# Kernel tuning notes

Measured on AMD Instinct MI355X. Metric: run time of the kernel, lower is better.

## Reference

```python
import jax, jax.numpy as jnp
import numpy as np

B, S, HID = 1, 2048, 2048
H, KVH, HD = 16, 8, 128          # query heads, kv heads, head_dim = HID//H
N_REP = H // KVH                 # GQA expansion factor
EPS = 1e-6
THETA = 1e6
SCALING = HD ** (-0.5)           # note: original DIVIDES scores by this (bug kept)


def setup_inputs() -> dict:
    key = jax.random.key(0)
    ks = jax.random.split(key, 5)
    hidden_states = jax.random.normal(ks[0], (B, S, HID), jnp.float32)
    std = 0.02
    wq = jax.random.normal(ks[1], (HID, H * HD), jnp.float32) * std
    wk = jax.random.normal(ks[2], (HID, KVH * HD), jnp.float32) * std
    wv = jax.random.normal(ks[3], (HID, KVH * HD), jnp.float32) * std
    wo = jax.random.normal(ks[4], (H * HD, HID), jnp.float32) * std
    # RoPE tables as in Qwen3: inv_freq over even dims, emb = [freqs, freqs]
    pos = np.arange(S, dtype=np.float64)
    inv_freq = THETA ** (-np.arange(0, HD, 2, dtype=np.float64) / HD)
    freqs = pos[:, None] * inv_freq[None, :]            # [S, HD/2]
    emb = np.concatenate([freqs, freqs], axis=-1)       # [S, HD]
    cos = jnp.asarray(np.cos(emb)[None], jnp.float32)   # [1, S, HD]
    sin = jnp.asarray(np.sin(emb)[None], jnp.float32)
    return {"hidden_states": hidden_states, "cos": cos, "sin": sin,
            "wq": wq, "wk": wk, "wv": wv, "wo": wo}


def _rmsnorm(x):
    # weightless RMSNorm (the module's RMSNorm never applies .weight)
    return x * jax.lax.rsqrt(jnp.mean(x * x, axis=-1, keepdims=True) + EPS)


def _rotate_half(x):
    x1, x2 = jnp.split(x, 2, axis=-1)
    return jnp.concatenate([-x2, x1], axis=-1)


def reference(hidden_states, cos, sin, wq, wk, wv, wo):
    # projections + per-head QK RMSNorm, then [B,H,S,D] layout
    q = _rmsnorm((hidden_states @ wq).reshape(B, S, H, HD)).transpose(0, 2, 1, 3)
    k = _rmsnorm((hidden_states @ wk).reshape(B, S, KVH, HD)).transpose(0, 2, 1, 3)
    v = (hidden_states @ wv).reshape(B, S, KVH, HD).transpose(0, 2, 1, 3)
    # RoPE (cos/sin unsqueezed at head dim)
    c = cos[:, None, :, :]   # [B,1,S,HD]
    s = sin[:, None, :, :]
    q = q * c + _rotate_half(q) * s
    k = k * c + _rotate_half(k) * s
    # GQA repeat_kv: each kv head repeated N_REP consecutive times
    k = jnp.repeat(k, N_REP, axis=1)   # [B,H,S,HD]
    v = jnp.repeat(v, N_REP, axis=1)
    # faithful: scores DIVIDED by head_dim**-0.5 (i.e. * sqrt(HD)); no causal mask
    scores = jnp.einsum('bhqd,bhkd->bhqk', q, k) / SCALING
    probs = jax.nn.softmax(scores, axis=-1)
    attn = jnp.einsum('bhqk,bhkd->bhqd', probs, v)
    out = attn.transpose(0, 2, 1, 3).reshape(B, S, H * HD) @ wo
    return out
```

## Files before the change

kernel.cpp:

```cpp
#include <hip/hip_runtime.h>
#include <hip/hip_bf16.h>
#include <math.h>

#define S 2048
#define HID 2048
#define NH 16
#define KVH 8
#define HD 128
#define EPS 1e-6f
#define QK_SCALE 11.313708498984760390f

typedef __attribute__((ext_vector_type(8))) short s16x8;
typedef __attribute__((ext_vector_type(4))) float f32x4;

__device__ __forceinline__ unsigned short f2bf(float f) {
  __hip_bfloat16 h = __float2bfloat16(f);
  return *(unsigned short*)&h;
}
__device__ __forceinline__ float bf2f(unsigned short u) {
  unsigned int x = ((unsigned int)u) << 16;
  return __builtin_bit_cast(float, x);
}

__device__ __forceinline__ void gload16(const void* g, void* l) {
  __builtin_amdgcn_global_load_lds(
      (const __attribute__((address_space(1))) void*)g,
      (__attribute__((address_space(3))) void*)l, 16, 0, 0);
}

__global__ __launch_bounds__(256) void f32_to_bf16_split(const float* __restrict__ in,
                                                         unsigned short* __restrict__ hi,
                                                         unsigned short* __restrict__ lo,
                                                         int n4) {
  const int i = blockIdx.x * 256 + threadIdx.x;
  if (i < n4) {
    const float4 v = *(const float4*)(in + (size_t)i * 4);
    ushort4 h, l;
    h.x = f2bf(v.x); l.x = f2bf(v.x - bf2f(h.x));
    h.y = f2bf(v.y); l.y = f2bf(v.y - bf2f(h.y));
    h.z = f2bf(v.z); l.z = f2bf(v.z - bf2f(h.z));
    h.w = f2bf(v.w); l.w = f2bf(v.w - bf2f(h.w));
    *(ushort4*)(hi + (size_t)i * 4) = h;
    *(ushort4*)(lo + (size_t)i * 4) = l;
  }
}

__global__ __launch_bounds__(256) void transpose_to_bf16(const float* __restrict__ in,
                                                         unsigned short* __restrict__ out,
                                                         int K, int N) {
  __shared__ float t[64][65];
  const int n0 = blockIdx.x * 64;
  const int k0 = blockIdx.y * 64;
  const int tid = threadIdx.x;

  for (int idx = tid; idx < 64 * 16; idx += 256) {
    const int r = idx >> 4;
    const int c4 = (idx & 15) * 4;
    const float4 v = *(const float4*)(in + (size_t)(k0 + r) * N + n0 + c4);
    t[r][c4 + 0] = v.x; t[r][c4 + 1] = v.y; t[r][c4 + 2] = v.z; t[r][c4 + 3] = v.w;
  }
  __syncthreads();
  for (int idx = tid; idx < 64 * 16; idx += 256) {
    const int a = idx >> 4;
    const int b4 = (idx & 15) * 4;
    ushort4 u;
    u.x = f2bf(t[b4 + 0][a]); u.y = f2bf(t[b4 + 1][a]);
    u.z = f2bf(t[b4 + 2][a]); u.w = f2bf(t[b4 + 3][a]);
    *(ushort4*)(out + (size_t)(n0 + a) * K + k0 + b4) = u;
  }
}

__global__ __launch_bounds__(256) void transpose_to_bf16_split(const float* __restrict__ in,
                                                               unsigned short* __restrict__ ohi,
                                                               unsigned short* __restrict__ olo,
                                                               int K, int N) {
  __shared__ float t[64][65];
  const int n0 = blockIdx.x * 64;
  const int k0 = blockIdx.y * 64;
  const int tid = threadIdx.x;

  for (int idx = tid; idx < 64 * 16; idx += 256) {
    const int r = idx >> 4;
    const int c4 = (idx & 15) * 4;
    const float4 v = *(const float4*)(in + (size_t)(k0 + r) * N + n0 + c4);
    t[r][c4 + 0] = v.x; t[r][c4 + 1] = v.y; t[r][c4 + 2] = v.z; t[r][c4 + 3] = v.w;
  }
  __syncthreads();
  for (int idx = tid; idx < 64 * 16; idx += 256) {
    const int a = idx >> 4;
    const int b4 = (idx & 15) * 4;
    ushort4 h, l;
#pragma unroll
    for (int q = 0; q < 4; ++q) {
      const float v = t[b4 + q][a];
      const unsigned short hu = f2bf(v);
      const unsigned short lu = f2bf(v - bf2f(hu));
      ((unsigned short*)&h)[q] = hu;
      ((unsigned short*)&l)[q] = lu;
    }
    *(ushort4*)(ohi + (size_t)(n0 + a) * K + k0 + b4) = h;
    *(ushort4*)(olo + (size_t)(n0 + a) * K + k0 + b4) = l;
  }
}

#define BM 128
#define BN 128
#define BK 32

template <typename OT>
__global__ __launch_bounds__(256) void gemm_bf16_bt(const unsigned short* __restrict__ A,
                                                    const unsigned short* __restrict__ Bt,
                                                    OT* __restrict__ C,
                                                    int M, int N, int K, int ldc) {
  __shared__ unsigned short As[BM * BK];
  __shared__ unsigned short Bs[BN * BK];

  const int tid = threadIdx.x;
  const int lane = tid & 63;
  const int wave = tid >> 6;
  const int m0 = blockIdx.y * BM;
  const int n0 = blockIdx.x * BN;

  const int qm = (wave >> 1) * 64;
  const int qn = (wave & 1) * 64;
  const int l15 = lane & 15;
  const int quad = lane >> 4;

  const int st_row = lane >> 2;
  const int st_col = (lane & 3) * 8;

  f32x4 acc[4][4] = {};

  for (int k0 = 0; k0 < K; k0 += BK) {
#pragma unroll
    for (int p = 0; p < 2; ++p) {
      const int rb = p * 64 + wave * 16;
      gload16(A + (size_t)(m0 + rb + st_row) * K + k0 + st_col, &As[rb * BK]);
      gload16(Bt + (size_t)(n0 + rb + st_row) * K + k0 + st_col, &Bs[rb * BK]);
    }
    __syncthreads();

    s16x8 a[4], b[4];
#pragma unroll
    for (int i = 0; i < 4; ++i)
      a[i] = *(const s16x8*)&As[(qm + i * 16 + l15) * BK + quad * 8];
#pragma unroll
    for (int j = 0; j < 4; ++j)
      b[j] = *(const s16x8*)&Bs[(qn + j * 16 + l15) * BK + quad * 8];
#pragma unroll
    for (int i = 0; i < 4; ++i)
#pragma unroll
      for (int j = 0; j < 4; ++j)
        acc[i][j] = __builtin_amdgcn_mfma_f32_16x16x32_bf16(a[i], b[j], acc[i][j], 0, 0, 0);
    __syncthreads();
  }

#pragma unroll
  for (int i = 0; i < 4; ++i) {
    const int row_base = m0 + qm + i * 16 + quad * 4;
#pragma unroll
    for (int j = 0; j < 4; ++j) {
      const int col = n0 + qn + j * 16 + l15;
#pragma unroll
      for (int r = 0; r < 4; ++r) {
        if constexpr (sizeof(OT) == 2)
          C[(size_t)(row_base + r) * ldc + col] = (OT)f2bf(acc[i][j][r]);
        else
          C[(size_t)(row_base + r) * ldc + col] = acc[i][j][r];
      }
    }
  }
}

template <int MODE, typename OT>
__global__ __launch_bounds__(256) void gemm_bf16_bt64(const unsigned short* __restrict__ A,
                                                      const unsigned short* __restrict__ Bt,
                                                      OT* __restrict__ C,
                                                      int M, int N, int K, int ldc) {
  __shared__ unsigned short As[BM * BK];
  __shared__ unsigned short Bs[64 * BK];

  const int tid = threadIdx.x;
  const int lane = tid & 63;
  const int wave = tid >> 6;
  const int m0 = blockIdx.y * BM;
  const int n0 = blockIdx.x * 64;

  const int qm = (wave >> 1) * 64;
  const int qn = (wave & 1) * 32;
  const int l15 = lane & 15;
  const int quad = lane >> 4;

  const int st_row = lane >> 2;
  const int st_col = (lane & 3) * 8;

  f32x4 acc[4][2] = {};

  for (int k0 = 0; k0 < K; k0 += BK) {
#pragma unroll
    for (int p = 0; p < 2; ++p) {
      const int rb = p * 64 + wave * 16;
      gload16(A + (size_t)(m0 + rb + st_row) * K + k0 + st_col, &As[rb * BK]);
    }
    {
      const int rb = wave * 16;
      gload16(Bt + (size_t)(n0 + rb + st_row) * K + k0 + st_col, &Bs[rb * BK]);
    }
    __syncthreads();

    s16x8 a[4], b[2];
#pragma unroll
    for (int i = 0; i < 4; ++i)
      a[i] = *(const s16x8*)&As[(qm + i * 16 + l15) * BK + quad * 8];
#pragma unroll
    for (int j = 0; j < 2; ++j)
      b[j] = *(const s16x8*)&Bs[(qn + j * 16 + l15) * BK + quad * 8];
#pragma unroll
    for (int i = 0; i < 4; ++i)
#pragma unroll
      for (int j = 0; j < 2; ++j)
        acc[i][j] = __builtin_amdgcn_mfma_f32_16x16x32_bf16(a[i], b[j], acc[i][j], 0, 0, 0);
    __syncthreads();
  }

#pragma unroll
  for (int i = 0; i < 4; ++i) {
    const int row_base = m0 + qm + i * 16 + quad * 4;
#pragma unroll
    for (int j = 0; j < 2; ++j) {
      const int col = n0 + qn + j * 16 + l15;
      if constexpr (MODE == 0) {
#pragma unroll
        for (int r = 0; r < 4; ++r)
          C[(size_t)(row_base + r) * ldc + col] = acc[i][j][r];
      } else {
        ushort4 u;
        u.x = f2bf(acc[i][j][0]); u.y = f2bf(acc[i][j][1]);
        u.z = f2bf(acc[i][j][2]); u.w = f2bf(acc[i][j][3]);
        *(ushort4*)((unsigned short*)C + (size_t)col * ldc + row_base) = u;
      }
    }
  }
}

__global__ __launch_bounds__(256) void gemm_split_bt(const unsigned short* __restrict__ Ahi,
                                                     const unsigned short* __restrict__ Alo,
                                                     const unsigned short* __restrict__ Bhi,
                                                     const unsigned short* __restrict__ Blo,
                                                     float* __restrict__ C,
                                                     int M, int N, int K, int ldc) {
  __shared__ unsigned short AsH[BM * BK];
  __shared__ unsigned short AsL[BM * BK];
  __shared__ unsigned short BsH[BN * BK];
  __shared__ unsigned short BsL[BN * BK];

  const int tid = threadIdx.x;
  const int lane = tid & 63;
  const int wave = tid >> 6;
  const int m0 = blockIdx.y * BM;
  const int n0 = blockIdx.x * BN;

  const int qm = (wave >> 1) * 64;
  const int qn = (wave & 1) * 64;
  const int l15 = lane & 15;
  const int quad = lane >> 4;

  const int st_row = lane >> 2;
  const int st_col = (lane & 3) * 8;

  f32x4 acc[4][4] = {};

  for (int k0 = 0; k0 < K; k0 += BK) {
#pragma unroll
    for (int p = 0; p < 2; ++p) {
      const int rb = p * 64 + wave * 16;
      const size_t aoff = (size_t)(m0 + rb + st_row) * K + k0 + st_col;
      const size_t boff = (size_t)(n0 + rb + st_row) * K + k0 + st_col;
      gload16(Ahi + aoff, &AsH[rb * BK]);
      gload16(Alo + aoff, &AsL[rb * BK]);
      gload16(Bhi + boff, &BsH[rb * BK]);
      gload16(Blo + boff, &BsL[rb * BK]);
    }
    __syncthreads();

    s16x8 ah[4], al[4], bh[4], bl[4];
#pragma unroll
    for (int i = 0; i < 4; ++i) {
      const int ro = (qm + i * 16 + l15) * BK + quad * 8;
      ah[i] = *(const s16x8*)&AsH[ro];
      al[i] = *(const s16x8*)&AsL[ro];
    }
#pragma unroll
    for (int j = 0; j < 4; ++j) {
      const int ro = (qn + j * 16 + l15) * BK + quad * 8;
      bh[j] = *(const s16x8*)&BsH[ro];
      bl[j] = *(const s16x8*)&BsL[ro];
    }
#pragma unroll
    for (int i = 0; i < 4; ++i)
#pragma unroll
      for (int j = 0; j < 4; ++j) {
        acc[i][j] = __builtin_amdgcn_mfma_f32_16x16x32_bf16(ah[i], bh[j], acc[i][j], 0, 0, 0);
        acc[i][j] = __builtin_amdgcn_mfma_f32_16x16x32_bf16(ah[i], bl[j], acc[i][j], 0, 0, 0);
        acc[i][j] = __builtin_amdgcn_mfma_f32_16x16x32_bf16(al[i], bh[j], acc[i][j], 0, 0, 0);
      }
    __syncthreads();
  }

#pragma unroll
  for (int i = 0; i < 4; ++i) {
    const int row_base = m0 + qm + i * 16 + quad * 4;
#pragma unroll
    for (int j = 0; j < 4; ++j) {
      const int col = n0 + qn + j * 16 + l15;
#pragma unroll
      for (int r = 0; r < 4; ++r)
        C[(size_t)(row_base + r) * ldc + col] = acc[i][j][r];
    }
  }
}

__global__ __launch_bounds__(256) void rmsnorm_rope_split(const float* __restrict__ qk,
                                                          const float* __restrict__ cosb,
                                                          const float* __restrict__ sinb,
                                                          unsigned short* __restrict__ qh,
                                                          unsigned short* __restrict__ ql,
                                                          unsigned short* __restrict__ kh,
                                                          unsigned short* __restrict__ kl) {
  const int s = blockIdx.x;
  const int wave = threadIdx.x >> 6;
  const int lane = threadIdx.x & 63;
  const int hh = blockIdx.y * 4 + wave;
  const bool is_q = (hh < 16);
  const int col = is_q ? hh * HD : 2048 + (hh - 16) * HD;

  const float* row = qk + (size_t)s * 3072 + col;
  const float x1 = row[lane];
  const float x2 = row[lane + 64];

  float ss = x1 * x1 + x2 * x2;
  ss += __shfl_xor(ss, 1);
  ss += __shfl_xor(ss, 2);
  ss += __shfl_xor(ss, 4);
  ss += __shfl_xor(ss, 8);
  ss += __shfl_xor(ss, 16);
  ss += __shfl_xor(ss, 32);
  const float r = rsqrtf(ss / 128.f + EPS);

  const float c = cosb[(size_t)s * HD + lane];
  const float sn = sinb[(size_t)s * HD + lane];
  float o1 = x1 * r * c - x2 * r * sn;
  float o2 = x2 * r * c + x1 * r * sn;
  if (is_q) { o1 *= QK_SCALE; o2 *= QK_SCALE; }

  const unsigned short h1 = f2bf(o1), l1 = f2bf(o1 - bf2f(h1));
  const unsigned short h2 = f2bf(o2), l2 = f2bf(o2 - bf2f(h2));
  if (is_q) {
    const size_t base = (size_t)s * 2048 + hh * HD + lane;
    qh[base] = h1; ql[base] = l1;
    qh[base + 64] = h2; ql[base + 64] = l2;
  } else {
    const size_t base = (size_t)s * 1024 + (hh - 16) * HD + lane;
    kh[base] = h1; kl[base] = l1;
    kh[base + 64] = h2; kl[base + 64] = l2;
  }
}

#define FA_N 64

__global__ __launch_bounds__(256, 2) void attn_flash_mfma(const unsigned short* __restrict__ qh,
                                                          const unsigned short* __restrict__ ql,
                                                          const unsigned short* __restrict__ kh,
                                                          const unsigned short* __restrict__ kl,
                                                          const unsigned short* __restrict__ vt,
                                                          unsigned short* __restrict__ out) {
  const int h = blockIdx.y;
  const int kvh = h >> 1;
  const int m0 = blockIdx.x * 64;
  const int tid = threadIdx.x;
  const int lane = tid & 63;
  const int wave = tid >> 6;
  const int rg = wave >> 1;
  const int kg = wave & 1;
  const int l15 = lane & 15;
  const int quad = lane >> 4;

  __shared__ char smem[59392];
  unsigned short* Kh = (unsigned short*)(smem);
  unsigned short* Kl = (unsigned short*)(smem + 16384);
  unsigned short* Vt = (unsigned short*)(smem + 32768);
  unsigned short* Pt = (unsigned short*)(smem + 49152) + wave * 1280;

  s16x8 qah[2][4], qal[2][4];
#pragma unroll
  for (int rt = 0; rt < 2; ++rt) {
    const int qrow = m0 + rg * 32 + rt * 16 + l15;
#pragma unroll
    for (int ks = 0; ks < 4; ++ks) {
      const size_t off = (size_t)qrow * 2048 + h * HD + ks * 32 + quad * 8;
      qah[rt][ks] = *(const s16x8*)(qh + off);
      qal[rt][ks] = *(const s16x8*)(ql + off);
    }
  }

  f32x4 O[2][8] = {};
  float m_i[2][4], l_i[2][4];
#pragma unroll
  for (int rt = 0; rt < 2; ++rt)
#pragma unroll
    for (int r = 0; r < 4; ++r) { m_i[rt][r] = -1e30f; l_i[rt][r] = 0.f; }

  for (int n0 = 0; n0 < S; n0 += FA_N) {
    __syncthreads();
#pragma unroll
    for (int p = 0; p < 4; ++p) {
      const int krow = wave * 16 + p * 4 + (lane >> 4);
      const int kc = (lane & 15) ^ (krow & 15);
      const size_t ksrc = (size_t)(n0 + krow) * 1024 + kvh * HD + kc * 8;
      const int kdst = (wave * 16 + p * 4) * 128;
      gload16(kh + ksrc, Kh + kdst);
      gload16(kl + ksrc, Kl + kdst);
      const int d = wave * 32 + p * 8 + (lane >> 3);
      const int vc = (lane & 7) ^ (d & 7);
      const size_t vsrc = (size_t)(kvh * HD + d) * 2048 + n0 + vc * 8;
      const int vdst = (wave * 32 + p * 8) * 64;
      gload16(vt + vsrc, Vt + vdst);
    }
    __syncthreads();

    f32x4 sacc[2][2] = {};
#pragma unroll
    for (int ks = 0; ks < 4; ++ks) {
      s16x8 bh[2], bl[2];
#pragma unroll
      for (int j = 0; j < 2; ++j) {
        const int row = kg * 32 + j * 16 + l15;
        const int cp = ((ks * 4 + quad) ^ l15) * 8;
        const int ro = row * 128 + cp;
        bh[j] = *(const s16x8*)&Kh[ro];
        bl[j] = *(const s16x8*)&Kl[ro];
      }
#pragma unroll
      for (int rt = 0; rt < 2; ++rt)
#pragma unroll
        for (int j = 0; j < 2; ++j) {
          sacc[rt][j] = __builtin_amdgcn_mfma_f32_16x16x32_bf16(qah[rt][ks], bh[j], sacc[rt][j], 0, 0, 0);
          sacc[rt][j] = __builtin_amdgcn_mfma_f32_16x16x32_bf16(qah[rt][ks], bl[j], sacc[rt][j], 0, 0, 0);
          sacc[rt][j] = __builtin_amdgcn_mfma_f32_16x16x32_bf16(qal[rt][ks], bh[j], sacc[rt][j], 0, 0, 0);
        }
    }

#pragma unroll
    for (int rt = 0; rt < 2; ++rt) {
#pragma unroll
      for (int r = 0; r < 4; ++r) {
        float mt = fmaxf(sacc[rt][0][r], sacc[rt][1][r]);
        mt = fmaxf(mt, __shfl_xor(mt, 1));
        mt = fmaxf(mt, __shfl_xor(mt, 2));
        mt = fmaxf(mt, __shfl_xor(mt, 4));
        mt = fmaxf(mt, __shfl_xor(mt, 8));
        const float mnew = fmaxf(m_i[rt][r], mt);
        const float alpha = __expf(m_i[rt][r] - mnew);
        m_i[rt][r] = mnew;
        const float p0 = __expf(sacc[rt][0][r] - mnew);
        const float p1 = __expf(sacc[rt][1][r] - mnew);
        l_i[rt][r] = l_i[rt][r] * alpha + (p0 + p1);
#pragma unroll
        for (int jd = 0; jd < 8; ++jd) O[rt][jd][r] *= alpha;
        const int prow = rt * 16 + quad * 4 + r;
        Pt[prow * 40 + l15] = f2bf(p0);
        Pt[prow * 40 + 16 + l15] = f2bf(p1);
      }
    }

    s16x8 pa[2];
#pragma unroll
    for (int rt = 0; rt < 2; ++rt)
      pa[rt] = *(const s16x8*)&Pt[(rt * 16 + l15) * 40 + quad * 8];
#pragma unroll
    for (int jd = 0; jd < 8; ++jd) {
      const int d = jd * 16 + l15;
      const int cp = ((kg * 4 + quad) ^ (d & 7)) * 8;
      const s16x8 vb = *(const s16x8*)&Vt[d * 64 + cp];
#pragma unroll
      for (int rt = 0; rt < 2; ++rt)
        O[rt][jd] = __builtin_amdgcn_mfma_f32_16x16x32_bf16(pa[rt], vb, O[rt][jd], 0, 0, 0);
    }
  }

#pragma unroll
  for (int rt = 0; rt < 2; ++rt)
#pragma unroll
    for (int r = 0; r < 4; ++r) {
      float ls = l_i[rt][r];
      ls += __shfl_xor(ls, 1);
      ls += __shfl_xor(ls, 2);
      ls += __shfl_xor(ls, 4);
      ls += __shfl_xor(ls, 8);
      l_i[rt][r] = ls;
    }

  __syncthreads();
  float* Om = (float*)smem;
  float* ms = (float*)(smem + 32768);
  float* ls2 = (float*)(smem + 33024);

  if (kg == 1) {
#pragma unroll
    for (int rt = 0; rt < 2; ++rt)
#pragma unroll
      for (int r = 0; r < 4; ++r) {
        const int row = rt * 16 + quad * 4 + r;
        if (l15 == 0) {
          ms[rg * 32 + row] = m_i[rt][r];
          ls2[rg * 32 + row] = l_i[rt][r];
        }
#pragma unroll
        for (int jd = 0; jd < 8; ++jd)
          Om[(size_t)(rg * 32 + row) * 128 + jd * 16 + l15] = O[rt][jd][r];
      }
  }
  __syncthreads();
  if (kg == 0) {
#pragma unroll
    for (int rt = 0; rt < 2; ++rt)
#pragma unroll
      for (int r = 0; r < 4; ++r) {
        const int row = rt * 16 + quad * 4 + r;
        const float mB = ms[rg * 32 + row];
        const float lB = ls2[rg * 32 + row];
        const float mS = fmaxf(m_i[rt][r], mB);
        const float aA = __expf(m_i[rt][r] - mS);
        const float aB = __expf(mB - mS);
        const float inv = 1.f / (aA * l_i[rt][r] + aB * lB);
        const int grow = m0 + rg * 32 + row;
#pragma unroll
        for (int jd = 0; jd < 8; ++jd) {
          const float oB = Om[(size_t)(rg * 32 + row) * 128 + jd * 16 + l15];
          out[(size_t)grow * 2048 + h * HD + jd * 16 + l15] =
              f2bf((aA * O[rt][jd][r] + aB * oB) * inv);
        }
      }
  }
}

extern "C" void kernel_launch(void* const* d_in, const int* in_sizes, int n_in,
                              void* d_out, int out_size, void* d_ws, size_t ws_size,
                              hipStream_t stream) {
  const float* hidden = (const float*)d_in[0];
  const float* cosb   = (const float*)d_in[1];
  const float* sinb   = (const float*)d_in[2];
  const float* wq     = (const float*)d_in[3];
  const float* wk     = (const float*)d_in[4];
  const float* wv     = (const float*)d_in[5];
  const float* wo     = (const float*)d_in[6];
  float* out = (float*)d_out;

  char* w = (char*)d_ws;
  float* qk_buf           = (float*)(w);
  unsigned short* wqkT_hi = (unsigned short*)(w + (24u << 20));
  unsigned short* wqkT_lo = (unsigned short*)(w + (36u << 20));
  unsigned short* hid_hi  = (unsigned short*)(w + (48u << 20));
  unsigned short* hid_lo  = (unsigned short*)(w + (56u << 20));
  unsigned short* vt_b    = (unsigned short*)(w + (64u << 20));
  unsigned short* wvT     = (unsigned short*)(w + (68u << 20));
  unsigned short* q_hi    = (unsigned short*)(w + (24u << 20));
  unsigned short* q_lo    = (unsigned short*)(w + (32u << 20));
  unsigned short* k_hi    = (unsigned short*)(w + (40u << 20));
  unsigned short* k_lo    = (unsigned short*)(w + (44u << 20));
  unsigned short* woT     = (unsigned short*)(w + (48u << 20));
  unsigned short* a_b     = (unsigned short*)(w + (56u << 20));

  dim3 blk(256);

  f32_to_bf16_split<<<dim3((S * HID / 4 + 255) / 256), blk, 0, stream>>>(hidden, hid_hi, hid_lo, S * HID / 4);
  transpose_to_bf16_split<<<dim3(32, 32), blk, 0, stream>>>(wq, wqkT_hi, wqkT_lo, HID, 2048);
  transpose_to_bf16_split<<<dim3(16, 32), blk, 0, stream>>>(wk, wqkT_hi + (size_t)2048 * 2048,
                                                            wqkT_lo + (size_t)2048 * 2048, HID, 1024);
  transpose_to_bf16<<<dim3(16, 32), blk, 0, stream>>>(wv, wvT, 2048, 1024);

  gemm_split_bt<<<dim3(3072 / BN, S / BM), blk, 0, stream>>>(hid_hi, hid_lo, wqkT_hi, wqkT_lo,
                                                             qk_buf, S, 3072, HID, 3072);

  gemm_bf16_bt64<1, unsigned short><<<dim3(1024 / 64, S / BM), blk, 0, stream>>>(
      hid_hi, wvT, vt_b, S, 1024, HID, 2048);

  transpose_to_bf16<<<dim3(32, 32), blk, 0, stream>>>(wo, woT, 2048, HID);

  rmsnorm_rope_split<<<dim3(S, 6), blk, 0, stream>>>(qk_buf, cosb, sinb, q_hi, q_lo, k_hi, k_lo);

  attn_flash_mfma<<<dim3(S / 64, NH), blk, 0, stream>>>(q_hi, q_lo, k_hi, k_lo, vt_b, a_b);

  gemm_bf16_bt64<0, float><<<dim3(HID / 64, S / BM), blk, 0, stream>>>(
      a_b, woT, out, S, HID, 2048, HID);
}
```

Baseline: 420.3 us.

## Prefetch next K/V tile into registers, add lazy softmax rescale and MFMA priority

The flash-attention loop now loads the next K/V tile from global memory into registers while the current tile's QK and PV MFMAs run, then writes it to LDS after a barrier. This replaces the synchronous direct-to-LDS load at the top of each iteration. The online softmax skips the running-max update and the O/l rescale unless some row's max grows by more than 8, which saves exp and multiply work. s_setprio is raised around the MFMA blocks. The prefetch costs extra VGPRs for the staged tiles, which can lower occupancy, and the lazy rescale lets exponents grow by up to e^8 before renormalisation.

```diff
diff --git a/kernel.cpp b/kernel.cpp
--- a/kernel.cpp
+++ b/kernel.cpp
@@ -391,6 +391,11 @@
   unsigned short* Vt = (unsigned short*)(smem + 32768);
   unsigned short* Pt = (unsigned short*)(smem + 49152) + wave * 1280;
 
+  const int krow = wave * 16 + (lane >> 4);
+  const int kc = (lane & 15);
+  const int vd = wave * 32 + (lane >> 3);
+  const int vc7 = (lane & 7);
+
   s16x8 qah[2][4], qal[2][4];
 #pragma unroll
   for (int rt = 0; rt < 2; ++rt) {
@@ -410,25 +415,39 @@
 #pragma unroll
     for (int r = 0; r < 4; ++r) { m_i[rt][r] = -1e30f; l_i[rt][r] = 0.f; }
 
+#pragma unroll
+  for (int p = 0; p < 4; ++p) {
+    const int kr = krow + p * 4;
+    const size_t ksrc = (size_t)kr * 1024 + kvh * HD + (kc ^ (kr & 15)) * 8;
+    const int kdst = (wave * 16 + p * 4) * 128;
+    gload16(kh + ksrc, Kh + kdst);
+    gload16(kl + ksrc, Kl + kdst);
+    const int d = vd + p * 8;
+    const size_t vsrc = (size_t)(kvh * HD + d) * 2048 + (vc7 ^ (d & 7)) * 8;
+    const int vdst = (wave * 32 + p * 8) * 64;
+    gload16(vt + vsrc, Vt + vdst);
+  }
+  __syncthreads();
+
   for (int n0 = 0; n0 < S; n0 += FA_N) {
-    __syncthreads();
-#pragma unroll
-    for (int p = 0; p < 4; ++p) {
-      const int krow = wave * 16 + p * 4 + (lane >> 4);
-      const int kc = (lane & 15) ^ (krow & 15);
-      const size_t ksrc = (size_t)(n0 + krow) * 1024 + kvh * HD + kc * 8;
-      const int kdst = (wave * 16 + p * 4) * 128;
-      gload16(kh + ksrc, Kh + kdst);
-      gload16(kl + ksrc, Kl + kdst);
-      const int d = wave * 32 + p * 8 + (lane >> 3);
-      const int vc = (lane & 7) ^ (d & 7);
-      const size_t vsrc = (size_t)(kvh * HD + d) * 2048 + n0 + vc * 8;
-      const int vdst = (wave * 32 + p * 8) * 64;
-      gload16(vt + vsrc, Vt + vdst);
-    }
-    __syncthreads();
+    const int n1 = n0 + FA_N;
+
+    s16x8 stKh[4], stKl[4], stV[4];
+    if (n1 < S) {
+#pragma unroll
+      for (int p = 0; p < 4; ++p) {
+        const int kr = krow + p * 4;
+        const size_t ksrc = (size_t)(n1 + kr) * 1024 + kvh * HD + (kc ^ (kr & 15)) * 8;
+        stKh[p] = *(const s16x8*)(kh + ksrc);
+        stKl[p] = *(const s16x8*)(kl + ksrc);
+        const int d = vd + p * 8;
+        const size_t vsrc = (size_t)(kvh * HD + d) * 2048 + n1 + (vc7 ^ (d & 7)) * 8;
+        stV[p] = *(const s16x8*)(vt + vsrc);
+      }
+    }
 
     f32x4 sacc[2][2] = {};
+    __builtin_amdgcn_s_setprio(1);
 #pragma unroll
     for (int ks = 0; ks < 4; ++ks) {
       s16x8 bh[2], bl[2];
@@ -449,34 +468,52 @@
           sacc[rt][j] = __builtin_amdgcn_mfma_f32_16x16x32_bf16(qal[rt][ks], bh[j], sacc[rt][j], 0, 0, 0);
         }
     }
-
-#pragma unroll
-    for (int rt = 0; rt < 2; ++rt) {
+    __builtin_amdgcn_s_setprio(0);
+
+    float mt[2][4];
+    float dmax = -1e30f;
+#pragma unroll
+    for (int rt = 0; rt < 2; ++rt)
 #pragma unroll
       for (int r = 0; r < 4; ++r) {
-        float mt = fmaxf(sacc[rt][0][r], sacc[rt][1][r]);
-        mt = fmaxf(mt, __shfl_xor(mt, 1));
-        mt = fmaxf(mt, __shfl_xor(mt, 2));
-        mt = fmaxf(mt, __shfl_xor(mt, 4));
-        mt = fmaxf(mt, __shfl_xor(mt, 8));
-        const float mnew = fmaxf(m_i[rt][r], mt);
-        const float alpha = __expf(m_i[rt][r] - mnew);
-        m_i[rt][r] = mnew;
-        const float p0 = __expf(sacc[rt][0][r] - mnew);
-        const float p1 = __expf(sacc[rt][1][r] - mnew);
-        l_i[rt][r] = l_i[rt][r] * alpha + (p0 + p1);
-#pragma unroll
-        for (int jd = 0; jd < 8; ++jd) O[rt][jd][r] *= alpha;
+        float m = fmaxf(sacc[rt][0][r], sacc[rt][1][r]);
+        m = fmaxf(m, __shfl_xor(m, 1));
+        m = fmaxf(m, __shfl_xor(m, 2));
+        m = fmaxf(m, __shfl_xor(m, 4));
+        m = fmaxf(m, __shfl_xor(m, 8));
+        mt[rt][r] = m;
+        dmax = fmaxf(dmax, m - m_i[rt][r]);
+      }
+    if (__any(dmax > 8.f)) {
+#pragma unroll
+      for (int rt = 0; rt < 2; ++rt)
+#pragma unroll
+        for (int r = 0; r < 4; ++r) {
+          const float mnew = fmaxf(m_i[rt][r], mt[rt][r]);
+          const float alpha = __expf(m_i[rt][r] - mnew);
+          m_i[rt][r] = mnew;
+          l_i[rt][r] *= alpha;
+#pragma unroll
+          for (int jd = 0; jd < 8; ++jd) O[rt][jd][r] *= alpha;
+        }
+    }
+#pragma unroll
+    for (int rt = 0; rt < 2; ++rt)
+#pragma unroll
+      for (int r = 0; r < 4; ++r) {
+        const float p0 = __expf(sacc[rt][0][r] - m_i[rt][r]);
+        const float p1 = __expf(sacc[rt][1][r] - m_i[rt][r]);
+        l_i[rt][r] += p0 + p1;
         const int prow = rt * 16 + quad * 4 + r;
         Pt[prow * 40 + l15] = f2bf(p0);
         Pt[prow * 40 + 16 + l15] = f2bf(p1);
       }
-    }
 
     s16x8 pa[2];
 #pragma unroll
     for (int rt = 0; rt < 2; ++rt)
       pa[rt] = *(const s16x8*)&Pt[(rt * 16 + l15) * 40 + quad * 8];
+    __builtin_amdgcn_s_setprio(1);
 #pragma unroll
     for (int jd = 0; jd < 8; ++jd) {
       const int d = jd * 16 + l15;
@@ -485,6 +522,20 @@
 #pragma unroll
       for (int rt = 0; rt < 2; ++rt)
         O[rt][jd] = __builtin_amdgcn_mfma_f32_16x16x32_bf16(pa[rt], vb, O[rt][jd], 0, 0, 0);
+    }
+    __builtin_amdgcn_s_setprio(0);
+
+    if (n1 < S) {
+      __syncthreads();
+#pragma unroll
+      for (int p = 0; p < 4; ++p) {
+        const int kdst = (wave * 16 + p * 4) * 128 + lane * 8;
+        *(s16x8*)&Kh[kdst] = stKh[p];
+        *(s16x8*)&Kl[kdst] = stKl[p];
+        const int vdst = (wave * 32 + p * 8) * 64 + lane * 8;
+        *(s16x8*)&Vt[vdst] = stV[p];
+      }
+      __syncthreads();
     }
   }
 
```

After: 526.0 us. 25.1% more time.

## Double-buffer K/V tiles in flash attention with 8-wave blocks and lazy rescaling

Applied to the files above, without the earlier changes.

The attention kernel moves to 512-thread blocks in which each wave owns 16 query rows. K/V tiles are double-buffered in LDS so the next tile's global-to-LDS copy is issued right after a single barrier and overlaps the current tile's math. The online-softmax rescale of O and l is now skipped unless some row's running max grows by more than 8. MFMA sections are wrapped in s_setprio to favour matrix issue. The ~106 KB LDS footprint probably limits the CU to one block, and the deferred rescale lets unnormalised probabilities reach about e^8 before they are rounded to bf16.

```diff
diff --git a/kernel.cpp b/kernel.cpp
--- a/kernel.cpp
+++ b/kernel.cpp
@@ -367,8 +367,9 @@
 }
 
 #define FA_N 64
-
-__global__ __launch_bounds__(256, 2) void attn_flash_mfma(const unsigned short* __restrict__ qh,
+#define FA_NT (S / FA_N)
+
+__global__ __launch_bounds__(512, 2) void attn_flash_mfma(const unsigned short* __restrict__ qh,
                                                           const unsigned short* __restrict__ ql,
                                                           const unsigned short* __restrict__ kh,
                                                           const unsigned short* __restrict__ kl,
@@ -385,120 +386,126 @@
   const int l15 = lane & 15;
   const int quad = lane >> 4;
 
-  __shared__ char smem[59392];
-  unsigned short* Kh = (unsigned short*)(smem);
-  unsigned short* Kl = (unsigned short*)(smem + 16384);
-  unsigned short* Vt = (unsigned short*)(smem + 32768);
-  unsigned short* Pt = (unsigned short*)(smem + 49152) + wave * 1280;
-
-  s16x8 qah[2][4], qal[2][4];
-#pragma unroll
-  for (int rt = 0; rt < 2; ++rt) {
-    const int qrow = m0 + rg * 32 + rt * 16 + l15;
+  __shared__ char smem[108544];
+  unsigned short* Pt = (unsigned short*)(smem + 98304) + wave * 640;
+
+  auto STAGE = [&](int nt, int buf) {
+    unsigned short* KhB = (unsigned short*)(smem + buf * 49152);
+    unsigned short* KlB = KhB + 8192;
+    unsigned short* VtB = KhB + 16384;
+#pragma unroll
+    for (int p = 0; p < 2; ++p) {
+      const int kr = wave * 8 + p * 4 + (lane >> 4);
+      const size_t ksrc = (size_t)(nt + kr) * 1024 + kvh * HD + ((lane & 15) ^ (kr & 15)) * 8;
+      gload16(kh + ksrc, KhB + (wave * 8 + p * 4) * 128);
+      gload16(kl + ksrc, KlB + (wave * 8 + p * 4) * 128);
+      const int d = wave * 16 + p * 8 + (lane >> 3);
+      const size_t vsrc = (size_t)(kvh * HD + d) * 2048 + nt + ((lane & 7) ^ (d & 7)) * 8;
+      gload16(vt + vsrc, VtB + (wave * 16 + p * 8) * 64);
+    }
+  };
+
+  s16x8 qah[4], qal[4];
+  {
+    const int qrow = m0 + rg * 16 + l15;
 #pragma unroll
     for (int ks = 0; ks < 4; ++ks) {
       const size_t off = (size_t)qrow * 2048 + h * HD + ks * 32 + quad * 8;
-      qah[rt][ks] = *(const s16x8*)(qh + off);
-      qal[rt][ks] = *(const s16x8*)(ql + off);
-    }
-  }
-
-  f32x4 O[2][8] = {};
-  float m_i[2][4], l_i[2][4];
-#pragma unroll
-  for (int rt = 0; rt < 2; ++rt)
-#pragma unroll
-    for (int r = 0; r < 4; ++r) { m_i[rt][r] = -1e30f; l_i[rt][r] = 0.f; }
-
-  for (int n0 = 0; n0 < S; n0 += FA_N) {
-    __syncthreads();
-#pragma unroll
-    for (int p = 0; p < 4; ++p) {
-      const int krow = wave * 16 + p * 4 + (lane >> 4);
-      const int kc = (lane & 15) ^ (krow & 15);
-      const size_t ksrc = (size_t)(n0 + krow) * 1024 + kvh * HD + kc * 8;
-      const int kdst = (wave * 16 + p * 4) * 128;
-      gload16(kh + ksrc, Kh + kdst);
-      gload16(kl + ksrc, Kl + kdst);
-      const int d = wave * 32 + p * 8 + (lane >> 3);
-      const int vc = (lane & 7) ^ (d & 7);
-      const size_t vsrc = (size_t)(kvh * HD + d) * 2048 + n0 + vc * 8;
-      const int vdst = (wave * 32 + p * 8) * 64;
-      gload16(vt + vsrc, Vt + vdst);
-    }
-    __syncthreads();
-
-    f32x4 sacc[2][2] = {};
+      qah[ks] = *(const s16x8*)(qh + off);
+      qal[ks] = *(const s16x8*)(ql + off);
+    }
+  }
+
+  f32x4 O[8] = {};
+  float m_i[4], l_i[4];
+#pragma unroll
+  for (int r = 0; r < 4; ++r) { m_i[r] = -1e30f; l_i[r] = 0.f; }
+
+  STAGE(0, 0);
+
+  for (int t = 0; t < FA_NT; ++t) {
+    unsigned short* Kh = (unsigned short*)(smem + (t & 1) * 49152);
+    unsigned short* Kl = Kh + 8192;
+    unsigned short* Vt = Kh + 16384;
+
+    __syncthreads();
+    if (t + 1 < FA_NT) STAGE((t + 1) * FA_N, (t + 1) & 1);
+
+    f32x4 sacc[2] = {};
+    __builtin_amdgcn_s_setprio(1);
 #pragma unroll
     for (int ks = 0; ks < 4; ++ks) {
       s16x8 bh[2], bl[2];
 #pragma unroll
       for (int j = 0; j < 2; ++j) {
         const int row = kg * 32 + j * 16 + l15;
-        const int cp = ((ks * 4 + quad) ^ l15) * 8;
-        const int ro = row * 128 + cp;
+        const int ro = row * 128 + (((ks * 4 + quad) ^ l15) * 8);
         bh[j] = *(const s16x8*)&Kh[ro];
         bl[j] = *(const s16x8*)&Kl[ro];
       }
 #pragma unroll
-      for (int rt = 0; rt < 2; ++rt)
-#pragma unroll
-        for (int j = 0; j < 2; ++j) {
-          sacc[rt][j] = __builtin_amdgcn_mfma_f32_16x16x32_bf16(qah[rt][ks], bh[j], sacc[rt][j], 0, 0, 0);
-          sacc[rt][j] = __builtin_amdgcn_mfma_f32_16x16x32_bf16(qah[rt][ks], bl[j], sacc[rt][j], 0, 0, 0);
-          sacc[rt][j] = __builtin_amdgcn_mfma_f32_16x16x32_bf16(qal[rt][ks], bh[j], sacc[rt][j], 0, 0, 0);
-        }
-    }
-
-#pragma unroll
-    for (int rt = 0; rt < 2; ++rt) {
+      for (int j = 0; j < 2; ++j) {
+        sacc[j] = __builtin_amdgcn_mfma_f32_16x16x32_bf16(qah[ks], bh[j], sacc[j], 0, 0, 0);
+        sacc[j] = __builtin_amdgcn_mfma_f32_16x16x32_bf16(qah[ks], bl[j], sacc[j], 0, 0, 0);
+        sacc[j] = __builtin_amdgcn_mfma_f32_16x16x32_bf16(qal[ks], bh[j], sacc[j], 0, 0, 0);
+      }
+    }
+    __builtin_amdgcn_s_setprio(0);
+
+    float mt[4];
+    float dmax = -1e30f;
+#pragma unroll
+    for (int r = 0; r < 4; ++r) {
+      float m = fmaxf(sacc[0][r], sacc[1][r]);
+      m = fmaxf(m, __shfl_xor(m, 1));
+      m = fmaxf(m, __shfl_xor(m, 2));
+      m = fmaxf(m, __shfl_xor(m, 4));
+      m = fmaxf(m, __shfl_xor(m, 8));
+      mt[r] = m;
+      dmax = fmaxf(dmax, m - m_i[r]);
+    }
+    if (__any(dmax > 8.f)) {
 #pragma unroll
       for (int r = 0; r < 4; ++r) {
-        float mt = fmaxf(sacc[rt][0][r], sacc[rt][1][r]);
-        mt = fmaxf(mt, __shfl_xor(mt, 1));
-        mt = fmaxf(mt, __shfl_xor(mt, 2));
-        mt = fmaxf(mt, __shfl_xor(mt, 4));
-        mt = fmaxf(mt, __shfl_xor(mt, 8));
-        const float mnew = fmaxf(m_i[rt][r], mt);
-        const float alpha = __expf(m_i[rt][r] - mnew);
-        m_i[rt][r] = mnew;
-        const float p0 = __expf(sacc[rt][0][r] - mnew);
-        const float p1 = __expf(sacc[rt][1][r] - mnew);
-        l_i[rt][r] = l_i[rt][r] * alpha + (p0 + p1);
-#pragma unroll
-        for (int jd = 0; jd < 8; ++jd) O[rt][jd][r] *= alpha;
-        const int prow = rt * 16 + quad * 4 + r;
-        Pt[prow * 40 + l15] = f2bf(p0);
-        Pt[prow * 40 + 16 + l15] = f2bf(p1);
-      }
-    }
-
-    s16x8 pa[2];
-#pragma unroll
-    for (int rt = 0; rt < 2; ++rt)
-      pa[rt] = *(const s16x8*)&Pt[(rt * 16 + l15) * 40 + quad * 8];
+        const float mnew = fmaxf(m_i[r], mt[r]);
+        const float alpha = __expf(m_i[r] - mnew);
+        m_i[r] = mnew;
+        l_i[r] *= alpha;
+#pragma unroll
+        for (int jd = 0; jd < 8; ++jd) O[jd][r] *= alpha;
+      }
+    }
+#pragma unroll
+    for (int r = 0; r < 4; ++r) {
+      const float p0 = __expf(sacc[0][r] - m_i[r]);
+      const float p1 = __expf(sacc[1][r] - m_i[r]);
+      l_i[r] += p0 + p1;
+      const int prow = quad * 4 + r;
+      Pt[prow * 40 + l15] = f2bf(p0);
+      Pt[prow * 40 + 16 + l15] = f2bf(p1);
+    }
+
+    const s16x8 pa = *(const s16x8*)&Pt[l15 * 40 + quad * 8];
+    __builtin_amdgcn_s_setprio(1);
 #pragma unroll
     for (int jd = 0; jd < 8; ++jd) {
       const int d = jd * 16 + l15;
       const int cp = ((kg * 4 + quad) ^ (d & 7)) * 8;
       const s16x8 vb = *(const s16x8*)&Vt[d * 64 + cp];
-#pragma unroll
-      for (int rt = 0; rt < 2; ++rt)
-        O[rt][jd] = __builtin_amdgcn_mfma_f32_16x16x32_bf16(pa[rt], vb, O[rt][jd], 0, 0, 0);
-    }
-  }
-
-#pragma unroll
-  for (int rt = 0; rt < 2; ++rt)
-#pragma unroll
-    for (int r = 0; r < 4; ++r) {
-      float ls = l_i[rt][r];
-      ls += __shfl_xor(ls, 1);
-      ls += __shfl_xor(ls, 2);
-      ls += __shfl_xor(ls, 4);
-      ls += __shfl_xor(ls, 8);
-      l_i[rt][r] = ls;
-    }
+      O[jd] = __builtin_amdgcn_mfma_f32_16x16x32_bf16(pa, vb, O[jd], 0, 0, 0);
+    }
+    __builtin_amdgcn_s_setprio(0);
+  }
+
+#pragma unroll
+  for (int r = 0; r < 4; ++r) {
+    float ls = l_i[r];
+    ls += __shfl_xor(ls, 1);
+    ls += __shfl_xor(ls, 2);
+    ls += __shfl_xor(ls, 4);
+    ls += __shfl_xor(ls, 8);
+    l_i[r] = ls;
+  }
 
   __syncthreads();
   float* Om = (float*)smem;
@@ -507,40 +514,33 @@
 
   if (kg == 1) {
 #pragma unroll
-    for (int rt = 0; rt < 2; ++rt)
-#pragma unroll
-      for (int r = 0; r < 4; ++r) {
-        const int row = rt * 16 + quad * 4 + r;
-        if (l15 == 0) {
-          ms[rg * 32 + row] = m_i[rt][r];
-          ls2[rg * 32 + row] = l_i[rt][r];
-        }
-#pragma unroll
-        for (int jd = 0; jd < 8; ++jd)
-          Om[(size_t)(rg * 32 + row) * 128 + jd * 16 + l15] = O[rt][jd][r];
-      }
+    for (int r = 0; r < 4; ++r) {
+      const int row = rg * 16 + quad * 4 + r;
+      if (l15 == 0) { ms[row] = m_i[r]; ls2[row] = l_i[r]; }
+#pragma unroll
+      for (int jd = 0; jd < 8; ++jd)
+        Om[(size_t)row * 128 + jd * 16 + l15] = O[jd][r];
+    }
   }
   __syncthreads();
   if (kg == 0) {
 #pragma unroll
-    for (int rt = 0; rt < 2; ++rt)
-#pragma unroll
-      for (int r = 0; r < 4; ++r) {
-        const int row = rt * 16 + quad * 4 + r;
-        const float mB = ms[rg * 32 + row];
-        const float lB = ls2[rg * 32 + row];
-        const float mS = fmaxf(m_i[rt][r], mB);
-        const float aA = __expf(m_i[rt][r] - mS);
-        const float aB = __expf(mB - mS);
-        const float inv = 1.f / (aA * l_i[rt][r] + aB * lB);
-        const int grow = m0 + rg * 32 + row;
-#pragma unroll
-        for (int jd = 0; jd < 8; ++jd) {
-          const float oB = Om[(size_t)(rg * 32 + row) * 128 + jd * 16 + l15];
-          out[(size_t)grow * 2048 + h * HD + jd * 16 + l15] =
-              f2bf((aA * O[rt][jd][r] + aB * oB) * inv);
-        }
-      }
+    for (int r = 0; r < 4; ++r) {
+      const int row = rg * 16 + quad * 4 + r;
+      const float mB = ms[row];
+      const float lB = ls2[row];
+      const float mS = fmaxf(m_i[r], mB);
+      const float aA = __expf(m_i[r] - mS);
+      const float aB = __expf(mB - mS);
+      const float inv = 1.f / (aA * l_i[r] + aB * lB);
+      const int grow = m0 + row;
+#pragma unroll
+      for (int jd = 0; jd < 8; ++jd) {
+        const float oB = Om[(size_t)row * 128 + jd * 16 + l15];
+        out[(size_t)grow * 2048 + h * HD + jd * 16 + l15] =
+            f2bf((aA * O[jd][r] + aB * oB) * inv);
+      }
+    }
   }
 }
 
@@ -589,7 +589,7 @@
 
   rmsnorm_rope_split<<<dim3(S, 6), blk, 0, stream>>>(qk_buf, cosb, sinb, q_hi, q_lo, k_hi, k_lo);
 
-  attn_flash_mfma<<<dim3(S / 64, NH), blk, 0, stream>>>(q_hi, q_lo, k_hi, k_lo, vt_b, a_b);
+  attn_flash_mfma<<<dim3(S / 64, NH), dim3(512), 0, stream>>>(q_hi, q_lo, k_hi, k_lo, vt_b, a_b);
 
   gemm_bf16_bt64<0, float><<<dim3(HID / 64, S / BM), blk, 0, stream>>>(
       a_b, woT, out, S, HID, 2048, HID);
```

Result: no change. 420.8 us (+0.1%).
